# Performance work log

Measured on AMD Instinct MI355X. Metric: run time of the kernel, lower is better.

Reference implementation:

```python
import jax, jax.numpy as jnp
import numpy as np

N = 16777216
C = 2
BINS = 10
MOMENTUM = 0.75


def setup_inputs() -> dict:
    key = jax.random.key(0)
    k1, k2 = jax.random.split(key)
    outputs = jax.random.normal(k1, (N, C), dtype=jnp.float32)
    targets = jax.random.randint(k2, (N,), 0, C, dtype=jnp.int64)
    acc_sum = jnp.zeros((BINS,), dtype=jnp.float32)
    return {"outputs": outputs, "targets": targets, "acc_sum": acc_sum}


def reference(outputs, targets, acc_sum):
    n, c = outputs.shape
    tgt = targets.astype(jnp.int32)
    logp = jax.nn.log_softmax(outputs, axis=1)            # [N, C]
    p_t = jnp.take_along_axis(jnp.exp(logp), tgt[:, None], axis=1)[:, 0]
    # |softmax - onehot| summed over classes == 2 * (1 - p_target)
    g = 2.0 * (1.0 - p_t)                                 # [N], in [0, 2]
    # torch loop covers edges linspace(0,1,bins+1): only g in [0, 1) gets a weight
    bin_idx = jnp.clip(jnp.floor(g * BINS).astype(jnp.int32), 0, BINS - 1)
    valid = g < 1.0
    counts = jax.ops.segment_sum(jnp.where(valid, 1.0, 0.0).astype(jnp.float32),
                                 bin_idx, num_segments=BINS)  # [BINS]
    # acc_sum updated only for non-empty bins (EMA with momentum)
    new_acc = jnp.where(counts > 0, MOMENTUM * acc_sum + (1.0 - MOMENTUM) * counts, acc_sum)
    per_sample_acc = new_acc[bin_idx]
    weights = jnp.where(valid & (counts[bin_idx] > 0),
                        jnp.float32(n) / per_sample_acc,
                        jnp.float32(0.0))                 # [N]
    # cross_entropy(reduction='none') = -log_softmax[target]
    loss = -jnp.take_along_axis(logp, tgt[:, None], axis=1)[:, 0]
    return jnp.mean(loss * weights)
```

## Files before the change

### kernel.cpp

```cpp
#include <hip/hip_runtime.h>

#define BINS   10
#define CSHIFT 26
#define QMASK  0x03FFFFFFu
#define QSCALE 2097152.0f
#define QLN2   1453635.25f
#define GRID   1536
#define TPB    256


__global__ void ghm_zero_ws(unsigned* ws) {
    if (threadIdx.x < 320) ws[threadIdx.x] = 0u;
}

__device__ __forceinline__ void gld_lds16_nt(const void* g, void* l) {
    __builtin_amdgcn_global_load_lds(
        (const __attribute__((address_space(1))) void*)g,
        (__attribute__((address_space(3))) void*)l, 16, 0, 2);
}

__device__ __forceinline__ void proc1(float o0, float o1, int t, unsigned* A) {
    const float Th[BINS] = {
        2.9444390f, 2.1972246f, 1.7346011f, 1.3862944f, 1.0986123f,
        0.8472979f, 0.6190392f, 0.4054651f, 0.2006707f, 0.0f };
    float s = o0 - o1;
    float d = __int_as_float(__float_as_int(s) ^ (t << 31));
    float em = __expf(-d);
    float qf = fmaf(__log2f(1.0f + em), QLN2, 0.5f);
    unsigned val = (unsigned)qf + (1u << CSHIFT);
    #pragma unroll
    for (int b = 0; b < BINS; ++b)
        A[b] += (d > Th[b]) ? val : 0u;
}

__global__ __launch_bounds__(TPB, 6)
void ghm_main(const float* __restrict__ outs,
              const int*   __restrict__ tgt,
              unsigned char* __restrict__ ws,
              int n, int use_slots) {
    __shared__ __align__(16) union {
        unsigned char ring[4][2][3072];
        struct {
            unsigned h[BINS][256];
            unsigned c[BINS][16];
            float    q[BINS][16];
        } ep;
    } sh;

    const int tid  = threadIdx.x;
    const int lane = tid & 63;
    const int wv   = tid >> 6;

    unsigned A[BINS];
    #pragma unroll
    for (int b = 0; b < BINS; ++b) A[b] = 0u;

    const int NT = n >> 8;
    const int NW = gridDim.x << 2;
    const int gw = (blockIdx.x << 2) + wv;

    const char* outs_b = (const char*)outs;
    const char* tgt_b  = (const char*)tgt;
    unsigned char* r0 = sh.ring[wv][0];
    unsigned char* r1 = sh.ring[wv][1];

    #define STAGE(tile, rp)                                                     \
        do {                                                                    \
            const char* go = outs_b + ((size_t)(tile) << 11) + (lane << 4);     \
            gld_lds16_nt(go,        (char*)(rp));                               \
            gld_lds16_nt(go + 1024, (char*)(rp) + 1024);                        \
            gld_lds16_nt(tgt_b + ((size_t)(tile) << 10) + (lane << 4),          \
                         (char*)(rp) + 2048);                                   \
        } while (0)

    int t = gw;
    if (t < NT) {
        STAGE(t, r0);
        int cur = 0;
        for (; t < NT; t += NW) {
            int tn = t + NW;
            if (tn >= NT) tn = 0;
            STAGE(tn, cur ? r0 : r1);
            asm volatile("s_waitcnt vmcnt(3)" ::: "memory");
            __builtin_amdgcn_sched_barrier(0);
            const unsigned char* rp = cur ? r1 : r0;
            const float4* o4 = (const float4*)rp;
            const int4*   t4 = (const int4*)(rp + 2048);
            float4 a  = o4[2 * lane];
            float4 bq = o4[2 * lane + 1];
            int4   tv = t4[lane];
            proc1(a.x,  a.y,  tv.x, A);
            proc1(a.z,  a.w,  tv.y, A);
            proc1(bq.x, bq.y, tv.z, A);
            proc1(bq.z, bq.w, tv.w, A);
            cur ^= 1;
        }
    }

    int rem = NT << 8;
    if (blockIdx.x == 0) {
        for (int s = rem + tid; s < n; s += TPB)
            proc1(outs[2 * s], outs[2 * s + 1], tgt[s], A);
    }

    __syncthreads();
    #pragma unroll
    for (int b = 0; b < BINS; ++b) sh.ep.h[b][tid] = A[b];
    __syncthreads();

    if (tid < 16 * BINS) {
        int bin  = tid >> 4;
        int part = tid & 15;
        unsigned c = 0, q = 0;
        #pragma unroll
        for (int j = 0; j < 16; ++j) {
            unsigned v = sh.ep.h[bin][j * 16 + part];
            c += v >> CSHIFT;
            q += v & QMASK;
        }
        sh.ep.c[bin][part] = c;
        sh.ep.q[bin][part] = (float)q;
    }
    __syncthreads();
    if (tid < BINS) {
        unsigned c = 0; float q = 0.0f;
        #pragma unroll
        for (int j = 0; j < 16; ++j) { c += sh.ep.c[tid][j]; q += sh.ep.q[tid][j]; }
        if (use_slots) {
            ((unsigned*)ws)[tid * GRID + blockIdx.x]        = c;
            ((float*)ws)[(BINS + tid) * GRID + blockIdx.x]  = q * (1.0f / QSCALE);
        } else if (c) {
            atomicAdd((unsigned*)(ws + 128 * tid + 64), c);
            atomicAdd((float*)   (ws + 128 * tid),      q * (1.0f / QSCALE));
        }
    }
}

__global__ __launch_bounds__(256)
void ghm_final2(const unsigned char* __restrict__ ws,
                const float* __restrict__ acc_sum,
                float* __restrict__ out) {
    __shared__ unsigned lc[BINS][256];
    __shared__ float    lq[BINS][256];
    __shared__ unsigned sc[BINS][16];
    __shared__ float    sq[BINS][16];
    const int tid = threadIdx.x;
    const unsigned* cb = (const unsigned*)ws;
    const float*    qb = (const float*)ws + (size_t)BINS * GRID;

    unsigned c[BINS]; float q[BINS];
    #pragma unroll
    for (int b = 0; b < BINS; ++b) { c[b] = 0u; q[b] = 0.0f; }
    for (int r = tid; r < GRID; r += 256) {
        #pragma unroll
        for (int b = 0; b < BINS; ++b) {
            c[b] += cb[b * GRID + r];
            q[b] += qb[b * GRID + r];
        }
    }
    #pragma unroll
    for (int b = 0; b < BINS; ++b) { lc[b][tid] = c[b]; lq[b][tid] = q[b]; }
    __syncthreads();

    if (tid < 16 * BINS) {
        int bin = tid >> 4, part = tid & 15;
        unsigned cc = 0u; float cq = 0.0f;
        #pragma unroll
        for (int j = 0; j < 16; ++j) {
            cc += lc[bin][j * 16 + part];
            cq += lq[bin][j * 16 + part];
        }
        sc[bin][part] = cc;
        sq[bin][part] = cq;
    }
    __syncthreads();

    if (tid == 0) {
        float r = 0.0f, pq = 0.0f;
        unsigned pc = 0u;
        #pragma unroll
        for (int b = 0; b < BINS; ++b) {
            unsigned cc = 0u; float cq = 0.0f;
            #pragma unroll
            for (int j = 0; j < 16; ++j) { cc += sc[b][j]; cq += sq[b][j]; }
            unsigned cnt = cc - pc;
            float    qs  = cq - pq;
            pc = cc; pq = cq;
            if (cnt > 0u) {
                float na = 0.75f * acc_sum[b] + 0.25f * (float)cnt;
                r += qs / na;
            }
        }
        *out = r;
    }
}

__global__ void ghm_final(const unsigned char* __restrict__ ws,
                          const float* __restrict__ acc_sum,
                          float* __restrict__ out) {
    if (threadIdx.x == 0) {
        float r = 0.0f, pq = 0.0f;
        unsigned pc = 0u;
        #pragma unroll
        for (int b = 0; b < BINS; ++b) {
            float    cq = *(const float*)   (ws + 128 * b);
            unsigned cc = *(const unsigned*)(ws + 128 * b + 64);
            unsigned cnt = cc - pc;
            float    qs  = cq - pq;
            pc = cc; pq = cq;
            if (cnt > 0u) {
                float na = 0.75f * acc_sum[b] + 0.25f * (float)cnt;
                r += qs / na;
            }
        }
        *out = r;
    }
}

extern "C" void kernel_launch(void* const* d_in, const int* in_sizes, int n_in,
                              void* d_out, int out_size, void* d_ws, size_t ws_size,
                              hipStream_t stream) {
    const float* outputs = (const float*)d_in[0];
    const int*   targets = (const int*)d_in[1];
    const float* acc_sum = (const float*)d_in[2];
    int n = in_sizes[1];

    const int use_slots = (ws_size >= (size_t)2 * BINS * GRID * 4) ? 1 : 0;

    if (!use_slots)
        ghm_zero_ws<<<1, 512, 0, stream>>>((unsigned*)d_ws);
    ghm_main<<<GRID, TPB, 0, stream>>>(outputs, targets,
                                       (unsigned char*)d_ws, n, use_slots);
    if (use_slots)
        ghm_final2<<<1, 256, 0, stream>>>((const unsigned char*)d_ws, acc_sum,
                                          (float*)d_out);
    else
        ghm_final<<<1, 64, 0, stream>>>((const unsigned char*)d_ws, acc_sum,
                                        (float*)d_out);
}
```

Measured before the change: 227.3 us.

## Replace LDS-staged global_load_lds ring with register double-buffered nontemporal loads

Drops the per-wave LDS ring fed by global_load_lds together with its manual vmcnt waits. Each thread now loads 16-byte outputs and targets vectors straight into registers using nontemporal loads, prefetching the next grid-stride element while it processes the current one. The grid grows from 1536 to 2048 blocks and launch bounds go to 8 waves per SIMD, which shrinks LDS use and raises occupancy. The risk is higher register pressure under the tighter bound, and the per-block slot workspace grows to match the larger grid.

```diff
diff --git a/kernel.cpp b/kernel.cpp
--- a/kernel.cpp
+++ b/kernel.cpp
@@ -5,7 +5,7 @@
 #define QMASK  0x03FFFFFFu
 #define QSCALE 2097152.0f
 #define QLN2   1453635.25f
-#define GRID   1536
+#define GRID   2048
 #define TPB    256
 
 
@@ -13,11 +13,11 @@
     if (threadIdx.x < 320) ws[threadIdx.x] = 0u;
 }
 
-__device__ __forceinline__ void gld_lds16_nt(const void* g, void* l) {
-    __builtin_amdgcn_global_load_lds(
-        (const __attribute__((address_space(1))) void*)g,
-        (__attribute__((address_space(3))) void*)l, 16, 0, 2);
-}
+typedef unsigned uv4 __attribute__((ext_vector_type(4)));
+__device__ __forceinline__ uv4 nt16(const void* p) {
+    return __builtin_nontemporal_load((const uv4*)p);
+}
+__device__ __forceinline__ float uf(unsigned u) { return __uint_as_float(u); }
 
 __device__ __forceinline__ void proc1(float o0, float o1, int t, unsigned* A) {
     const float Th[BINS] = {
@@ -33,79 +33,58 @@
         A[b] += (d > Th[b]) ? val : 0u;
 }
 
-__global__ __launch_bounds__(TPB, 6)
+__global__ __launch_bounds__(TPB, 8)
 void ghm_main(const float* __restrict__ outs,
               const int*   __restrict__ tgt,
               unsigned char* __restrict__ ws,
               int n, int use_slots) {
-    __shared__ __align__(16) union {
-        unsigned char ring[4][2][3072];
-        struct {
-            unsigned h[BINS][256];
-            unsigned c[BINS][16];
-            float    q[BINS][16];
-        } ep;
-    } sh;
-
-    const int tid  = threadIdx.x;
-    const int lane = tid & 63;
-    const int wv   = tid >> 6;
+    __shared__ unsigned h[BINS][TPB];
+    __shared__ unsigned sc[BINS][16];
+    __shared__ float    sq[BINS][16];
+
+    const int tid = threadIdx.x;
 
     unsigned A[BINS];
     #pragma unroll
     for (int b = 0; b < BINS; ++b) A[b] = 0u;
 
-    const int NT = n >> 8;
-    const int NW = gridDim.x << 2;
-    const int gw = (blockIdx.x << 2) + wv;
-
-    const char* outs_b = (const char*)outs;
-    const char* tgt_b  = (const char*)tgt;
-    unsigned char* r0 = sh.ring[wv][0];
-    unsigned char* r1 = sh.ring[wv][1];
-
-    #define STAGE(tile, rp)                                                     \
-        do {                                                                    \
-            const char* go = outs_b + ((size_t)(tile) << 11) + (lane << 4);     \
-            gld_lds16_nt(go,        (char*)(rp));                               \
-            gld_lds16_nt(go + 1024, (char*)(rp) + 1024);                        \
-            gld_lds16_nt(tgt_b + ((size_t)(tile) << 10) + (lane << 4),          \
-                         (char*)(rp) + 2048);                                   \
-        } while (0)
-
-    int t = gw;
-    if (t < NT) {
-        STAGE(t, r0);
-        int cur = 0;
-        for (; t < NT; t += NW) {
-            int tn = t + NW;
-            if (tn >= NT) tn = 0;
-            STAGE(tn, cur ? r0 : r1);
-            asm volatile("s_waitcnt vmcnt(3)" ::: "memory");
-            __builtin_amdgcn_sched_barrier(0);
-            const unsigned char* rp = cur ? r1 : r0;
-            const float4* o4 = (const float4*)rp;
-            const int4*   t4 = (const int4*)(rp + 2048);
-            float4 a  = o4[2 * lane];
-            float4 bq = o4[2 * lane + 1];
-            int4   tv = t4[lane];
-            proc1(a.x,  a.y,  tv.x, A);
-            proc1(a.z,  a.w,  tv.y, A);
-            proc1(bq.x, bq.y, tv.z, A);
-            proc1(bq.z, bq.w, tv.w, A);
-            cur ^= 1;
-        }
-    }
-
-    int rem = NT << 8;
+    const int nq = n >> 2;
+    const int stride = gridDim.x * TPB;
+    const uv4* __restrict__ o4 = (const uv4*)outs;
+    const uv4* __restrict__ t4 = (const uv4*)tgt;
+
+    int i = blockIdx.x * TPB + tid;
+    bool have = i < nq;
+    uv4 a0 = {}, b0 = {}, t0 = {};
+    uv4 a1 = {}, b1 = {}, t1 = {};
+    if (have) {
+        a0 = nt16(o4 + 2 * (size_t)i);
+        b0 = nt16(o4 + 2 * (size_t)i + 1);
+        t0 = nt16(t4 + i);
+    }
+    while (have) {
+        const int  i1    = i + stride;
+        const bool have1 = i1 < nq;
+        if (have1) {
+            a1 = nt16(o4 + 2 * (size_t)i1);
+            b1 = nt16(o4 + 2 * (size_t)i1 + 1);
+            t1 = nt16(t4 + i1);
+        }
+        proc1(uf(a0.x), uf(a0.y), (int)t0.x, A);
+        proc1(uf(a0.z), uf(a0.w), (int)t0.y, A);
+        proc1(uf(b0.x), uf(b0.y), (int)t0.z, A);
+        proc1(uf(b0.z), uf(b0.w), (int)t0.w, A);
+        a0 = a1; b0 = b1; t0 = t1;
+        i = i1; have = have1;
+    }
+
     if (blockIdx.x == 0) {
-        for (int s = rem + tid; s < n; s += TPB)
+        for (int s = (nq << 2) + tid; s < n; s += TPB)
             proc1(outs[2 * s], outs[2 * s + 1], tgt[s], A);
     }
 
-    __syncthreads();
-    #pragma unroll
-    for (int b = 0; b < BINS; ++b) sh.ep.h[b][tid] = A[b];
+    #pragma unroll
+    for (int b = 0; b < BINS; ++b) h[b][tid] = A[b];
     __syncthreads();
 
     if (tid < 16 * BINS) {
@@ -114,18 +93,18 @@
         unsigned c = 0, q = 0;
         #pragma unroll
         for (int j = 0; j < 16; ++j) {
-            unsigned v = sh.ep.h[bin][j * 16 + part];
+            unsigned v = h[bin][j * 16 + part];
             c += v >> CSHIFT;
             q += v & QMASK;
         }
-        sh.ep.c[bin][part] = c;
-        sh.ep.q[bin][part] = (float)q;
+        sc[bin][part] = c;
+        sq[bin][part] = (float)q;
     }
     __syncthreads();
     if (tid < BINS) {
         unsigned c = 0; float q = 0.0f;
         #pragma unroll
-        for (int j = 0; j < 16; ++j) { c += sh.ep.c[tid][j]; q += sh.ep.q[tid][j]; }
+        for (int j = 0; j < 16; ++j) { c += sc[tid][j]; q += sq[tid][j]; }
         if (use_slots) {
             ((unsigned*)ws)[tid * GRID + blockIdx.x]        = c;
             ((float*)ws)[(BINS + tid) * GRID + blockIdx.x]  = q * (1.0f / QSCALE);
```

Result: no change. 225.5 us (-0.8%).
